# Optimization experiments

Measured on AMD Instinct MI355X. Metric: run time of the kernel, lower is better.

The kernel has to match this reference:

```python
import jax, jax.numpy as jnp
import numpy as np

D = 128
H = 128  # scorer hidden

def setup_inputs() -> dict:
    key = jax.random.key(0)
    ks = jax.random.split(key, 8)
    B, T = 4096, 200
    transformer_out = jax.random.normal(ks[0], (B, T, D), dtype=jnp.float32)
    candidate = jax.random.normal(ks[1], (B, D), dtype=jnp.float32)
    mask = jax.random.randint(ks[2], (B, T), 0, 2).astype(jnp.bool_)
    # scorer params: Linear(3D,H) -> PReLU -> Linear(H,1)
    lim1 = 1.0 / np.sqrt(3 * D)
    W1 = jax.random.uniform(ks[3], (3 * D, H), minval=-lim1, maxval=lim1, dtype=jnp.float32)
    b1 = jax.random.uniform(ks[4], (H,), minval=-lim1, maxval=lim1, dtype=jnp.float32)
    a = jnp.array(0.25, dtype=jnp.float32)  # PReLU default init
    lim2 = 1.0 / np.sqrt(H)
    W2 = jax.random.uniform(ks[5], (H, 1), minval=-lim2, maxval=lim2, dtype=jnp.float32)
    b2 = jax.random.uniform(ks[6], (1,), minval=-lim2, maxval=lim2, dtype=jnp.float32)
    return {"transformer_out": transformer_out, "candidate": candidate, "mask": mask,
            "W1": W1, "b1": b1, "a": a, "W2": W2, "b2": b2}

def reference(transformer_out, candidate, mask, W1, b1, a, W2, b2):
    # transformer_out: [B,T,D], candidate: [B,D]
    cand_exp = jnp.broadcast_to(candidate[:, None, :], transformer_out.shape)  # [B,T,D]
    att_input = jnp.concatenate([transformer_out, cand_exp, transformer_out * cand_exp], axis=-1)  # [B,T,3D]
    h = att_input @ W1 + b1                       # [B,T,H]
    h = jnp.where(h >= 0, h, a * h)               # PReLU (single shared alpha)
    scores = (h @ W2 + b2)[..., 0]                # [B,T]
    scores = jnp.where(mask, scores, -jnp.inf)
    weights = jax.nn.softmax(scores, axis=-1)     # [B,T]
    return jnp.einsum('bt,btd->bd', weights, transformer_out)  # [B,D]
```

## Files before the change

kernel.cpp:

```cpp
#include <hip/hip_runtime.h>
#include <hip/hip_bf16.h>

typedef __attribute__((ext_vector_type(8))) short short8;
typedef __attribute__((ext_vector_type(4))) float f32x4;

#define B_T 200
#define B_D 128

static __device__ __forceinline__ short f2bf(float f) {
  unsigned u = __builtin_bit_cast(unsigned, f);
  u += 0x7fffu + ((u >> 16) & 1u);
  return (short)(u >> 16);
}
static __device__ __forceinline__ short8 cvt8(f32x4 a, f32x4 b) {
  short8 t;
  t[0] = f2bf(a[0]); t[1] = f2bf(a[1]); t[2] = f2bf(a[2]); t[3] = f2bf(a[3]);
  t[4] = f2bf(b[0]); t[5] = f2bf(b[1]); t[6] = f2bf(b[2]); t[7] = f2bf(b[3]);
  return t;
}

__global__ __launch_bounds__(256)
__attribute__((amdgpu_waves_per_eu(4, 4)))
void ta_fused(const float* __restrict__ x,
              const float* __restrict__ cand,
              const void*  __restrict__ maskp,
              const float* __restrict__ W1,
              const float* __restrict__ b1,
              const float* __restrict__ ap,
              const float* __restrict__ W2,
              const float* __restrict__ b2p,
              float* __restrict__ out)
{
  __shared__ __align__(16) short wbt[B_D * B_D];
  __shared__ float part[8][B_D];
  __shared__ float scores[208];
  __shared__ float red[8];

  const int b    = blockIdx.x;
  const int tid  = threadIdx.x;
  const int lane = tid & 63;
  const int wv   = tid >> 6;
  const int l15  = lane & 15;
  const int g    = lane >> 4;

  const float* xr0p = x + ((size_t)b * B_T + wv * 16 + l15) * B_D + g * 8;
  f32x4 r0 = *(const f32x4*)(xr0p +  0), r1 = *(const f32x4*)(xr0p +   4);
  f32x4 r2 = *(const f32x4*)(xr0p + 32), r3 = *(const f32x4*)(xr0p +  36);
  f32x4 r4 = *(const f32x4*)(xr0p + 64), r5 = *(const f32x4*)(xr0p +  68);
  f32x4 r6 = *(const f32x4*)(xr0p + 96), r7 = *(const f32x4*)(xr0p + 100);

  int flag1b;
  {
    const unsigned char* mb = (const unsigned char*)maskp;
    unsigned long long v8 = *(const unsigned long long*)(mb + lane * 8);
    flag1b = __any((v8 & 0xFFFFFF00FFFFFF00ull) != 0ull);
  }
  bool mk = false;
  if (tid < B_T) {
    if (flag1b) mk = ((const unsigned char*)maskp)[(size_t)b * B_T + tid] != 0;
    else        mk = ((const int*)maskp)[(size_t)b * B_T + tid] != 0;
  }

  const float* cb = cand + (size_t)b * B_D;
  {
    const int j = tid & 127;
    const int h = tid >> 7;
    #pragma unroll 2
    for (int it = 0; it < 8; ++it) {
      const int ko = it * 2 + h, k0 = ko * 8;
      short8 t;
      #pragma unroll
      for (int e = 0; e < 8; ++e) {
        float c  = cb[k0 + e];
        float wa = W1[(size_t)(k0 + e) * B_D + j];
        float wc = W1[(size_t)(256 + k0 + e) * B_D + j];
        t[e] = f2bf(fmaf(c, wc, wa));
      }
      *(short8*)&wbt[(ko * B_D + j) * 8] = t;
    }
    float s0 = (h == 0) ? b1[j] : 0.f, s1 = 0.f, s2 = 0.f, s3 = 0.f;
    const float* w1b = W1 + (size_t)(B_D + h * 64) * B_D + j;
    #pragma unroll 8
    for (int k = 0; k < 64; k += 4) {
      s0 = fmaf(cb[h * 64 + k    ], w1b[(size_t)(k    ) * B_D], s0);
      s1 = fmaf(cb[h * 64 + k + 1], w1b[(size_t)(k + 1) * B_D], s1);
      s2 = fmaf(cb[h * 64 + k + 2], w1b[(size_t)(k + 2) * B_D], s2);
      s3 = fmaf(cb[h * 64 + k + 3], w1b[(size_t)(k + 3) * B_D], s3);
    }
    part[h][j] = (s0 + s1) + (s2 + s3);
  }
  __syncthreads();

  float betaL[8], w2L[8];
  #pragma unroll
  for (int nt = 0; nt < 8; ++nt) {
    int col = nt * 16 + l15;
    betaL[nt] = part[0][col] + part[1][col];
    w2L[nt]   = W2[col];
  }
  const float alpha = ap[0];

#define LOADX(MT_ROW) do {                                                    \
    const float* xp_ = x + ((size_t)b * B_T + (MT_ROW)) * B_D + g * 8;        \
    r0 = *(const f32x4*)(xp_ +  0); r1 = *(const f32x4*)(xp_ +   4);          \
    r2 = *(const f32x4*)(xp_ + 32); r3 = *(const f32x4*)(xp_ +  36);          \
    r4 = *(const f32x4*)(xp_ + 64); r5 = *(const f32x4*)(xp_ +  68);          \
    r6 = *(const f32x4*)(xp_ + 96); r7 = *(const f32x4*)(xp_ + 100);          \
  } while (0)

#define COMPUTE_SCORE(TB) do {                                                \
    float sc[4] = {0.f, 0.f, 0.f, 0.f};                                       \
    _Pragma("unroll")                                                         \
    for (int nt = 0; nt < 8; ++nt) {                                          \
      f32x4 acc = {0.f, 0.f, 0.f, 0.f};                                       \
      const short8* wp = (const short8*)wbt + g * B_D + nt * 16 + l15;        \
      acc = __builtin_amdgcn_mfma_f32_16x16x32_bf16(a0, wp[0],    acc, 0,0,0);\
      acc = __builtin_amdgcn_mfma_f32_16x16x32_bf16(a1, wp[512],  acc, 0,0,0);\
      acc = __builtin_amdgcn_mfma_f32_16x16x32_bf16(a2, wp[1024], acc, 0,0,0);\
      acc = __builtin_amdgcn_mfma_f32_16x16x32_bf16(a3, wp[1536], acc, 0,0,0);\
      _Pragma("unroll")                                                       \
      for (int r = 0; r < 4; ++r) {                                           \
        float h_ = acc[r] + betaL[nt];                                        \
        float p_ = (h_ >= 0.f) ? h_ : alpha * h_;                             \
        sc[r] += p_ * w2L[nt];                                                \
      }                                                                       \
    }                                                                         \
    _Pragma("unroll")                                                         \
    for (int r = 0; r < 4; ++r) {                                             \
      float v = sc[r];                                                        \
      v += __shfl_xor(v, 1, 16); v += __shfl_xor(v, 2, 16);                   \
      v += __shfl_xor(v, 4, 16); v += __shfl_xor(v, 8, 16);                   \
      if (l15 == 0) scores[(TB) + g * 4 + r] = v;                             \
    }                                                                         \
  } while (0)

  short8 a0 = cvt8(r0, r1), a1 = cvt8(r2, r3), a2 = cvt8(r4, r5), a3 = cvt8(r6, r7);
  LOADX((4 + wv) * 16 + l15);
  COMPUTE_SCORE(wv * 16);

  a0 = cvt8(r0, r1); a1 = cvt8(r2, r3); a2 = cvt8(r4, r5); a3 = cvt8(r6, r7);
  LOADX((8 + wv) * 16 + l15);
  COMPUTE_SCORE((4 + wv) * 16);

  a0 = cvt8(r0, r1); a1 = cvt8(r2, r3); a2 = cvt8(r4, r5); a3 = cvt8(r6, r7);
  if (wv == 0) {
    int row3 = 192 + l15; if (row3 > B_T - 1) row3 = B_T - 1;
    LOADX(row3);
  }
  COMPUTE_SCORE((8 + wv) * 16);

  if (wv == 0) {
    a0 = cvt8(r0, r1); a1 = cvt8(r2, r3); a2 = cvt8(r4, r5); a3 = cvt8(r6, r7);
    COMPUTE_SCORE(192);
  }
#undef LOADX
#undef COMPUTE_SCORE
  __syncthreads();

  {
    float s = (tid < B_T && mk) ? scores[tid] : -INFINITY;
    float v = s;
    #pragma unroll
    for (int m = 32; m >= 1; m >>= 1) v = fmaxf(v, __shfl_xor(v, m, 64));
    if (lane == 0) red[wv] = v;
    __syncthreads();
    float mx = fmaxf(fmaxf(red[0], red[1]), fmaxf(red[2], red[3]));
    float e = mk ? __expf(s - mx) : 0.f;
    float sv = e;
    #pragma unroll
    for (int m = 32; m >= 1; m >>= 1) sv += __shfl_xor(sv, m, 64);
    if (lane == 0) red[4 + wv] = sv;
    if (tid < 208) scores[tid] = e;
    __syncthreads();
  }

  {
    const int d4 = (tid & 31) << 2;
    const int p  = tid >> 5;
    const float* xc = x + ((size_t)b * B_T + p * 25) * B_D + d4;
    f32x4 acc0 = {0.f, 0.f, 0.f, 0.f}, acc1 = {0.f, 0.f, 0.f, 0.f};
    #pragma unroll
    for (int t = 0; t < 24; t += 2) {
      f32x4 xv0 = *(const f32x4*)(xc + (size_t)t * B_D);
      f32x4 xv1 = *(const f32x4*)(xc + (size_t)(t + 1) * B_D);
      float w0 = scores[p * 25 + t];
      float w1 = scores[p * 25 + t + 1];
      acc0[0] = fmaf(w0, xv0[0], acc0[0]); acc1[0] = fmaf(w1, xv1[0], acc1[0]);
      acc0[1] = fmaf(w0, xv0[1], acc0[1]); acc1[1] = fmaf(w1, xv1[1], acc1[1]);
      acc0[2] = fmaf(w0, xv0[2], acc0[2]); acc1[2] = fmaf(w1, xv1[2], acc1[2]);
      acc0[3] = fmaf(w0, xv0[3], acc0[3]); acc1[3] = fmaf(w1, xv1[3], acc1[3]);
    }
    {
      f32x4 xv = *(const f32x4*)(xc + (size_t)24 * B_D);
      float w = scores[p * 25 + 24];
      acc0[0] = fmaf(w, xv[0], acc0[0]); acc0[1] = fmaf(w, xv[1], acc0[1]);
      acc0[2] = fmaf(w, xv[2], acc0[2]); acc0[3] = fmaf(w, xv[3], acc0[3]);
    }
    acc0[0] += acc1[0]; acc0[1] += acc1[1]; acc0[2] += acc1[2]; acc0[3] += acc1[3];
    *(f32x4*)&part[p][d4] = acc0;
  }
  __syncthreads();
  if (tid < B_D) {
    float Z = (red[4] + red[5]) + (red[6] + red[7]);
    float s = 0.f;
    #pragma unroll
    for (int p = 0; p < 8; ++p) s += part[p][tid];
    out[(size_t)b * B_D + tid] = s / Z;
  }
}

extern "C" void kernel_launch(void* const* d_in, const int* in_sizes, int n_in,
                              void* d_out, int out_size, void* d_ws, size_t ws_size,
                              hipStream_t stream) {
  const float* x    = (const float*)d_in[0];
  const float* cand = (const float*)d_in[1];
  const void*  mask = d_in[2];
  const float* W1   = (const float*)d_in[3];
  const float* b1   = (const float*)d_in[4];
  const float* a    = (const float*)d_in[5];
  const float* W2   = (const float*)d_in[6];
  const float* b2   = (const float*)d_in[7];
  float* out = (float*)d_out;
  const int B = in_sizes[1] / B_D;
  ta_fused<<<B, 256, 0, stream>>>(x, cand, mask, W1, b1, a, W2, b2, out);
}
```

Before: 147.5 us.

## Keep W1 B-fragments in registers, split N across waves, stage X through LDS

Each wave now keeps its 32-column slice of the folded W1 weights in registers as bf16 MFMA fragments instead of one 32KB LDS matrix. Every wave walks all 13 row tiles of the sequence. The block stages X tiles through a small triple-buffered padded LDS buffer with prefetch two tiles ahead. Per-wave partial scores are summed before the softmax. This cuts LDS use so occupancy can rise (waves_per_eu 4→5) and drops repeated B-operand LDS reads. The cost is a __syncthreads per tile and serialized per-tile staging.

Result: slower. 384.0 us (+160.3%).

```diff
diff --git a/kernel.cpp b/kernel.cpp
--- a/kernel.cpp
+++ b/kernel.cpp
@@ -6,6 +6,7 @@
 
 #define B_T 200
 #define B_D 128
+#define ALD 136
 
 static __device__ __forceinline__ short f2bf(float f) {
   unsigned u = __builtin_bit_cast(unsigned, f);
@@ -20,7 +21,7 @@
 }
 
 __global__ __launch_bounds__(256)
-__attribute__((amdgpu_waves_per_eu(4, 4)))
+__attribute__((amdgpu_waves_per_eu(5, 5)))
 void ta_fused(const float* __restrict__ x,
               const float* __restrict__ cand,
               const void*  __restrict__ maskp,
@@ -31,9 +32,10 @@
               const float* __restrict__ b2p,
               float* __restrict__ out)
 {
-  __shared__ __align__(16) short wbt[B_D * B_D];
+  __shared__ __align__(16) short a_lds[3][16 * ALD];
+  __shared__ float sp[4][208];
+  __shared__ float scores[208];
   __shared__ float part[8][B_D];
-  __shared__ float scores[208];
   __shared__ float red[8];
 
   const int b    = blockIdx.x;
@@ -42,12 +44,6 @@
   const int wv   = tid >> 6;
   const int l15  = lane & 15;
   const int g    = lane >> 4;
-
-  const float* xr0p = x + ((size_t)b * B_T + wv * 16 + l15) * B_D + g * 8;
-  f32x4 r0 = *(const f32x4*)(xr0p +  0), r1 = *(const f32x4*)(xr0p +   4);
-  f32x4 r2 = *(const f32x4*)(xr0p + 32), r3 = *(const f32x4*)(xr0p +  36);
-  f32x4 r4 = *(const f32x4*)(xr0p + 64), r5 = *(const f32x4*)(xr0p +  68);
-  f32x4 r6 = *(const f32x4*)(xr0p + 96), r7 = *(const f32x4*)(xr0p + 100);
 
   int flag1b;
   {
@@ -61,111 +57,85 @@
     else        mk = ((const int*)maskp)[(size_t)b * B_T + tid] != 0;
   }
 
+#define STAGE(MT, BUF) do {                                                   \
+    int srow_ = (MT) * 16 + (tid >> 4);                                       \
+    if (srow_ > B_T - 1) srow_ = B_T - 1;                                     \
+    const float* xp_ = x + ((size_t)b * B_T + srow_) * B_D + (tid & 15) * 8;  \
+    f32x4 v0_ = *(const f32x4*)xp_;                                           \
+    f32x4 v1_ = *(const f32x4*)(xp_ + 4);                                     \
+    *(short8*)&a_lds[BUF][(tid >> 4) * ALD + (tid & 15) * 8] = cvt8(v0_, v1_);\
+  } while (0)
+
+  STAGE(0, 0);
+  STAGE(1, 1);
+
   const float* cb = cand + (size_t)b * B_D;
+  const int j0 = wv * 32 + l15, j1 = j0 + 16;
+  short8 B0[4], B1[4];
+  #pragma unroll
+  for (int ks = 0; ks < 4; ++ks) {
+    short8 t0, t1;
+    #pragma unroll
+    for (int e = 0; e < 8; ++e) {
+      const int k = ks * 32 + g * 8 + e;
+      float c = cb[k];
+      t0[e] = f2bf(fmaf(c, W1[(size_t)(256 + k) * B_D + j0], W1[(size_t)k * B_D + j0]));
+      t1[e] = f2bf(fmaf(c, W1[(size_t)(256 + k) * B_D + j1], W1[(size_t)k * B_D + j1]));
+    }
+    B0[ks] = t0; B1[ks] = t1;
+  }
+  float betaL0, betaL1;
   {
-    const int j = tid & 127;
-    const int h = tid >> 7;
-    #pragma unroll 2
-    for (int it = 0; it < 8; ++it) {
-      const int ko = it * 2 + h, k0 = ko * 8;
-      short8 t;
-      #pragma unroll
-      for (int e = 0; e < 8; ++e) {
-        float c  = cb[k0 + e];
-        float wa = W1[(size_t)(k0 + e) * B_D + j];
-        float wc = W1[(size_t)(256 + k0 + e) * B_D + j];
-        t[e] = f2bf(fmaf(c, wc, wa));
-      }
-      *(short8*)&wbt[(ko * B_D + j) * 8] = t;
+    float s0 = 0.f, s1 = 0.f;
+    #pragma unroll 8
+    for (int kk = 0; kk < 32; ++kk) {
+      const int k = g * 32 + kk;
+      float c = cb[k];
+      s0 = fmaf(c, W1[(size_t)(B_D + k) * B_D + j0], s0);
+      s1 = fmaf(c, W1[(size_t)(B_D + k) * B_D + j1], s1);
     }
-    float s0 = (h == 0) ? b1[j] : 0.f, s1 = 0.f, s2 = 0.f, s3 = 0.f;
-    const float* w1b = W1 + (size_t)(B_D + h * 64) * B_D + j;
-    #pragma unroll 8
-    for (int k = 0; k < 64; k += 4) {
-      s0 = fmaf(cb[h * 64 + k    ], w1b[(size_t)(k    ) * B_D], s0);
-      s1 = fmaf(cb[h * 64 + k + 1], w1b[(size_t)(k + 1) * B_D], s1);
-      s2 = fmaf(cb[h * 64 + k + 2], w1b[(size_t)(k + 2) * B_D], s2);
-      s3 = fmaf(cb[h * 64 + k + 3], w1b[(size_t)(k + 3) * B_D], s3);
-    }
-    part[h][j] = (s0 + s1) + (s2 + s3);
+    s0 += __shfl_xor(s0, 16, 64); s0 += __shfl_xor(s0, 32, 64);
+    s1 += __shfl_xor(s1, 16, 64); s1 += __shfl_xor(s1, 32, 64);
+    betaL0 = s0 + b1[j0];
+    betaL1 = s1 + b1[j1];
   }
+  const float w2L0 = W2[j0], w2L1 = W2[j1];
+  const float alpha = ap[0];
   __syncthreads();
 
-  float betaL[8], w2L[8];
-  #pragma unroll
-  for (int nt = 0; nt < 8; ++nt) {
-    int col = nt * 16 + l15;
-    betaL[nt] = part[0][col] + part[1][col];
-    w2L[nt]   = W2[col];
+  for (int mt = 0; mt < 13; ++mt) {
+    const int buf = mt % 3;
+    if (mt + 2 < 13) STAGE(mt + 2, (mt + 2) % 3);
+    f32x4 acc0 = {0.f, 0.f, 0.f, 0.f}, acc1 = {0.f, 0.f, 0.f, 0.f};
+    #pragma unroll
+    for (int ks = 0; ks < 4; ++ks) {
+      short8 a = *(const short8*)&a_lds[buf][l15 * ALD + ks * 32 + g * 8];
+      acc0 = __builtin_amdgcn_mfma_f32_16x16x32_bf16(a, B0[ks], acc0, 0, 0, 0);
+      acc1 = __builtin_amdgcn_mfma_f32_16x16x32_bf16(a, B1[ks], acc1, 0, 0, 0);
+    }
+    #pragma unroll
+    for (int r = 0; r < 4; ++r) {
+      float h0 = acc0[r] + betaL0; h0 = (h0 >= 0.f) ? h0 : alpha * h0;
+      float h1 = acc1[r] + betaL1; h1 = (h1 >= 0.f) ? h1 : alpha * h1;
+      float v = h0 * w2L0 + h1 * w2L1;
+      v += __shfl_xor(v, 1, 16); v += __shfl_xor(v, 2, 16);
+      v += __shfl_xor(v, 4, 16); v += __shfl_xor(v, 8, 16);
+      if (l15 == 0) sp[wv][mt * 16 + g * 4 + r] = v;
+    }
+    __syncthreads();
   }
-  const float alpha = ap[0];
-
-#define LOADX(MT_ROW) do {                                                    \
-    const float* xp_ = x + ((size_t)b * B_T + (MT_ROW)) * B_D + g * 8;        \
-    r0 = *(const f32x4*)(xp_ +  0); r1 = *(const f32x4*)(xp_ +   4);          \
-    r2 = *(const f32x4*)(xp_ + 32); r3 = *(const f32x4*)(xp_ +  36);          \
-    r4 = *(const f32x4*)(xp_ + 64); r5 = *(const f32x4*)(xp_ +  68);          \
-    r6 = *(const f32x4*)(xp_ + 96); r7 = *(const f32x4*)(xp_ + 100);          \
-  } while (0)
-
-#define COMPUTE_SCORE(TB) do {                                                \
-    float sc[4] = {0.f, 0.f, 0.f, 0.f};                                       \
-    _Pragma("unroll")                                                         \
-    for (int nt = 0; nt < 8; ++nt) {                                          \
-      f32x4 acc = {0.f, 0.f, 0.f, 0.f};                                       \
-      const short8* wp = (const short8*)wbt + g * B_D + nt * 16 + l15;        \
-      acc = __builtin_amdgcn_mfma_f32_16x16x32_bf16(a0, wp[0],    acc, 0,0,0);\
-      acc = __builtin_amdgcn_mfma_f32_16x16x32_bf16(a1, wp[512],  acc, 0,0,0);\
-      acc = __builtin_amdgcn_mfma_f32_16x16x32_bf16(a2, wp[1024], acc, 0,0,0);\
-      acc = __builtin_amdgcn_mfma_f32_16x16x32_bf16(a3, wp[1536], acc, 0,0,0);\
-      _Pragma("unroll")                                                       \
-      for (int r = 0; r < 4; ++r) {                                           \
-        float h_ = acc[r] + betaL[nt];                                        \
-        float p_ = (h_ >= 0.f) ? h_ : alpha * h_;                             \
-        sc[r] += p_ * w2L[nt];                                                \
-      }                                                                       \
-    }                                                                         \
-    _Pragma("unroll")                                                         \
-    for (int r = 0; r < 4; ++r) {                                             \
-      float v = sc[r];                                                        \
-      v += __shfl_xor(v, 1, 16); v += __shfl_xor(v, 2, 16);                   \
-      v += __shfl_xor(v, 4, 16); v += __shfl_xor(v, 8, 16);                   \
-      if (l15 == 0) scores[(TB) + g * 4 + r] = v;                             \
-    }                                                                         \
-  } while (0)
-
-  short8 a0 = cvt8(r0, r1), a1 = cvt8(r2, r3), a2 = cvt8(r4, r5), a3 = cvt8(r6, r7);
-  LOADX((4 + wv) * 16 + l15);
-  COMPUTE_SCORE(wv * 16);
-
-  a0 = cvt8(r0, r1); a1 = cvt8(r2, r3); a2 = cvt8(r4, r5); a3 = cvt8(r6, r7);
-  LOADX((8 + wv) * 16 + l15);
-  COMPUTE_SCORE((4 + wv) * 16);
-
-  a0 = cvt8(r0, r1); a1 = cvt8(r2, r3); a2 = cvt8(r4, r5); a3 = cvt8(r6, r7);
-  if (wv == 0) {
-    int row3 = 192 + l15; if (row3 > B_T - 1) row3 = B_T - 1;
-    LOADX(row3);
-  }
-  COMPUTE_SCORE((8 + wv) * 16);
-
-  if (wv == 0) {
-    a0 = cvt8(r0, r1); a1 = cvt8(r2, r3); a2 = cvt8(r4, r5); a3 = cvt8(r6, r7);
-    COMPUTE_SCORE(192);
-  }
-#undef LOADX
-#undef COMPUTE_SCORE
-  __syncthreads();
+#undef STAGE
 
   {
-    float s = (tid < B_T && mk) ? scores[tid] : -INFINITY;
+    float s = -INFINITY;
+    if (tid < B_T && mk) s = (sp[0][tid] + sp[1][tid]) + (sp[2][tid] + sp[3][tid]);
     float v = s;
     #pragma unroll
     for (int m = 32; m >= 1; m >>= 1) v = fmaxf(v, __shfl_xor(v, m, 64));
     if (lane == 0) red[wv] = v;
     __syncthreads();
     float mx = fmaxf(fmaxf(red[0], red[1]), fmaxf(red[2], red[3]));
-    float e = mk ? __expf(s - mx) : 0.f;
+    float e = (tid < B_T && mk) ? __expf(s - mx) : 0.f;
     float sv = e;
     #pragma unroll
     for (int m = 32; m >= 1; m >>= 1) sv += __shfl_xor(sv, m, 64);
```
